# Kernel optimization log

Measured on AMD Instinct MI355X. Metric: run time of the kernel, lower is better.

The kernel has to match this reference:

```python
import jax, jax.numpy as jnp
import numpy as np

LN_EPS = 1e-5  # torch nn.LayerNorm default eps


def _layernorm(x, g, b):
    m = jnp.mean(x, -1, keepdims=True)
    v = jnp.mean((x - m) ** 2, -1, keepdims=True)
    return (x - m) / jnp.sqrt(v + LN_EPS) * g + b


def _dw_causal_conv(x, w, bias=None):
    # x: (B, L, C); w: (C, K) depthwise kernels; causal via left-pad K-1
    C = x.shape[-1]
    K = w.shape[-1]
    xt = jnp.swapaxes(x, 1, 2)                       # (B, C, L)
    xp = jnp.pad(xt, ((0, 0), (0, 0), (K - 1, 0)))
    y = jax.lax.conv_general_dilated(
        xp, w[:, None, :], (1,), 'VALID',
        feature_group_count=C, dimension_numbers=('NCH', 'OIH', 'NCH'))
    if bias is not None:
        y = y + bias[None, :, None]
    return jnp.swapaxes(y, 1, 2)                     # (B, L, C)


def _s4d(x, Bp, Cp, log_dt, Dp):
    # Diagonal SSM: kernel K[l] = sum_n C[n]*dB[n]*dA[n]^l, shared across channels
    L, Dm = x.shape[1], x.shape[2]
    n = Bp.shape[0]
    A = -jnp.arange(1, n + 1, dtype=x.dtype)
    dt = jnp.clip(jnp.exp(log_dt), 1e-4, 1.0)
    dA = jnp.exp(jnp.clip(dt * A, -10.0, 10.0))                  # (n,)
    dB = (dA - 1.0) / jnp.minimum(A, -1e-4) * Bp                 # (n,)
    pows = dA[:, None] ** jnp.arange(L, dtype=x.dtype)[None, :]  # (n, L)
    Kk = jnp.nan_to_num((Cp * dB) @ pows, nan=0.0, posinf=0.0, neginf=0.0)  # (L,)
    y = _dw_causal_conv(x, jnp.broadcast_to(Kk[None, :], (Dm, L)))
    return y + Dp * x


def _mamba_block(x, g, b, W_in, cw, cb, sB, sC, ldt, sD, W_out, rs):
    res = x
    h = _layernorm(x, g, b)
    xz = h @ W_in.T                                  # (B, L, 2*d_inner)
    xp, z = jnp.split(xz, 2, axis=-1)
    xc = _dw_causal_conv(xp, cw, cb)                 # depthwise causal conv, k=4
    y = _s4d(xc, sB, sC, ldt, sD) * jax.nn.sigmoid(z)
    y = y @ W_out.T
    return res + jnp.clip(rs, 0.0, 1.5) * y          # dropout is identity in eval


def _forward(spatial_tokens_init, pos_embed, ln_g, ln_b, W_in, conv_w, conv_b,
             ssm_B, ssm_C, log_dt, ssm_D, W_out, res_scale, fin_g, fin_b,
             imp_W1, imp_b1, imp_W2, imp_b2, tex_W, tex_b, edge_W, edge_b,
             str_W, str_b):
    x = spatial_tokens_init + pos_embed
    for i in range(ln_g.shape[0]):  # fixed small layer count
        x = _mamba_block(x, ln_g[i], ln_b[i], W_in[i], conv_w[i], conv_b[i],
                         ssm_B[i], ssm_C[i], log_dt[i], ssm_D[i], W_out[i],
                         res_scale[i])
    tokens = _layernorm(x, fin_g, fin_b)
    # F.normalize(dim=-1, eps=1e-6)
    tn = tokens / jnp.maximum(jnp.sqrt(jnp.sum(tokens ** 2, -1, keepdims=True)), 1e-6)
    h = jax.nn.gelu(tn @ imp_W1.T + imp_b1, approximate=False)
    logits = (h @ imp_W2.T + imp_b2)[..., 0]
    w = jax.nn.softmax(logits, axis=-1)
    feats = jnp.sum(tokens * w[..., None], axis=1)
    return (feats,
            feats @ tex_W.T + tex_b,
            feats @ edge_W.T + edge_b,
            feats @ str_W.T + str_b,
            tokens, w)


B, N, D, DI, NL, NS, KC, DH = 512, 256, 128, 256, 4, 16, 4, 64
H = D // 2


def setup_inputs() -> dict:
    ks = jax.random.split(jax.random.key(0), 26)
    r = lambda k, sh, s=0.02: jax.random.normal(k, sh, dtype=jnp.float32) * s
    inp = {
        'spatial_tokens_init': jax.random.normal(ks[0], (B, N, D), dtype=jnp.float32),
        'pos_embed': r(ks[1], (1, N, D)),
        'ln_g': jnp.ones((NL, D), jnp.float32),
        'ln_b': jnp.zeros((NL, D), jnp.float32),
        'W_in': r(ks[2], (NL, 2 * DI, D)),
        'conv_w': r(ks[3], (NL, DI, KC), 0.2),
        'conv_b': r(ks[4], (NL, DI), 0.02),
        'ssm_B': r(ks[5], (NL, NS)),
        'ssm_C': r(ks[6], (NL, NS)),
        'log_dt': jax.random.uniform(ks[7], (NL,), jnp.float32,
                                     minval=float(np.log(1e-3)), maxval=float(np.log(0.1))),
        'ssm_D': jnp.zeros((NL,), jnp.float32),
        'W_out': r(ks[8], (NL, D, DI)),
        'res_scale': jnp.ones((NL,), jnp.float32),
        'fin_g': jnp.ones((D,), jnp.float32),
        'fin_b': jnp.zeros((D,), jnp.float32),
        'imp_W1': r(ks[9], (H, D)),
        'imp_b1': jnp.zeros((H,), jnp.float32),
        'imp_W2': r(ks[10], (1, H)),
        'imp_b2': jnp.zeros((1,), jnp.float32),
        'tex_W': r(ks[11], (DH, D)),
        'tex_b': jnp.zeros((DH,), jnp.float32),
        'edge_W': r(ks[12], (DH, D)),
        'edge_b': jnp.zeros((DH,), jnp.float32),
        'str_W': r(ks[13], (DH, D)),
        'str_b': jnp.zeros((DH,), jnp.float32),
    }
    return inp


def reference(spatial_tokens_init, pos_embed, ln_g, ln_b, W_in, conv_w, conv_b,
              ssm_B, ssm_C, log_dt, ssm_D, W_out, res_scale, fin_g, fin_b,
              imp_W1, imp_b1, imp_W2, imp_b2, tex_W, tex_b, edge_W, edge_b,
              str_W, str_b):
    return _forward(spatial_tokens_init, pos_embed, ln_g, ln_b, W_in, conv_w,
                    conv_b, ssm_B, ssm_C, log_dt, ssm_D, W_out, res_scale,
                    fin_g, fin_b, imp_W1, imp_b1, imp_W2, imp_b2, tex_W, tex_b,
                    edge_W, edge_b, str_W, str_b)
```

## Files before the change

### kernel.cpp

```cpp
#include <hip/hip_runtime.h>
#include <hip/hip_bf16.h>


typedef __bf16 bf16_8 __attribute__((ext_vector_type(8)));
typedef __bf16 bf16_4 __attribute__((ext_vector_type(4)));
typedef float  f32_4  __attribute__((ext_vector_type(4)));

#define GLOAD16(src, dst) __builtin_amdgcn_global_load_lds( \
    (const __attribute__((address_space(1))) void*)(src),   \
    (__attribute__((address_space(3))) void*)(dst), 16, 0, 0)

__device__ __forceinline__ float fsig(float z) {
    float e = __expf(-z);
    return __builtin_amdgcn_rcpf(1.0f + e);
}

__global__ __launch_bounds__(256) void prep_kernel(const float* __restrict__ win,
                                                   const float* __restrict__ wout,
                                                   const float* __restrict__ w1,
                                                   __bf16* __restrict__ win16,
                                                   __bf16* __restrict__ wout16,
                                                   __bf16* __restrict__ w116) {
    int i = blockIdx.x * 256 + threadIdx.x;
    if (i < 4 * 512 * 128) win16[i] = (__bf16)win[i];
    if (i < 4 * 128 * 256) wout16[i] = (__bf16)wout[i];
    if (i < 64 * 128)      w116[i]  = (__bf16)w1[i];
}

__global__ __launch_bounds__(256) void build_T_kernel(const float* __restrict__ Bp,
                                                      const float* __restrict__ Cp,
                                                      const float* __restrict__ ldt,
                                                      const float* __restrict__ Dpv,
                                                      __bf16* __restrict__ Tg,
                                                      float* __restrict__ Rg) {
    __shared__ float rsum[4];
    int layer = blockIdx.y, l = blockIdx.x, j = threadIdx.x;
    int d = l - j;
    float val = 0.0f;
    if (d >= 0) {
        float dt = expf(ldt[layer]);
        dt = fminf(fmaxf(dt, 1e-4f), 1.0f);
        #pragma unroll
        for (int n = 0; n < 16; ++n) {
            float A = -(float)(n + 1);
            float e = fminf(fmaxf(dt * A, -10.0f), 10.0f);
            float dA = expf(e);
            float dB = (dA - 1.0f) / A * Bp[layer * 16 + n];
            val += Cp[layer * 16 + n] * dB * expf(e * (float)d);
        }
        if (d == 0) val += Dpv[layer];
    }
    __bf16 bv = (__bf16)val;
    Tg[layer * 65536 + l * 256 + j] = bv;
    float fv = (float)bv;
    #pragma unroll
    for (int o = 32; o; o >>= 1) fv += __shfl_xor(fv, o);
    int lane = j & 63, wave = j >> 6;
    if (lane == 0) rsum[wave] = fv;
    __syncthreads();
    if (j == 0) Rg[layer * 256 + l] = rsum[0] + rsum[1] + rsum[2] + rsum[3];
}

__global__ __launch_bounds__(256) void ln_first_kernel(const float4* __restrict__ init4,
                                                       const float4* __restrict__ pos4,
                                                       const float* __restrict__ g,
                                                       const float* __restrict__ bta,
                                                       float4* __restrict__ x4,
                                                       __bf16* __restrict__ h) {
    int tid = threadIdx.x;
    int wave = tid >> 6, lane = tid & 63;
    int half = lane >> 5, l32 = lane & 31;
    long tok = (long)blockIdx.x * 8 + wave * 2 + half;
    float4 v = init4[tok * 32 + l32];
    float4 p = pos4[(tok & 255) * 32 + l32];
    v.x += p.x; v.y += p.y; v.z += p.z; v.w += p.w;
    x4[tok * 32 + l32] = v;
    float s = v.x + v.y + v.z + v.w;
    float ss = v.x * v.x + v.y * v.y + v.z * v.z + v.w * v.w;
    #pragma unroll
    for (int o = 16; o; o >>= 1) { s += __shfl_xor(s, o); ss += __shfl_xor(ss, o); }
    float m = s * (1.0f / 128.0f);
    float var = ss * (1.0f / 128.0f) - m * m;
    float r = rsqrtf(var + 1e-5f);
    bf16_4 hv;
    int d0 = l32 * 4;
    hv[0] = (__bf16)((v.x - m) * r * g[d0]     + bta[d0]);
    hv[1] = (__bf16)((v.y - m) * r * g[d0 + 1] + bta[d0 + 1]);
    hv[2] = (__bf16)((v.z - m) * r * g[d0 + 2] + bta[d0 + 2]);
    hv[3] = (__bf16)((v.w - m) * r * g[d0 + 3] + bta[d0 + 3]);
    *(bf16_4*)(h + tok * 128 + d0) = hv;
}

__global__ __launch_bounds__(256) void gemm1_kernel(const __bf16* __restrict__ hmat,
                                                    const __bf16* __restrict__ win,
                                                    __bf16* __restrict__ xpt,
                                                    __bf16* __restrict__ z) {
    __shared__ __align__(16) __bf16 As[128 * 64];
    __shared__ __align__(16) __bf16 Bs[128 * 64];
    int tid = threadIdx.x;
    long m0 = (long)blockIdx.x * 128;
    int n0 = blockIdx.y * 128;
    int wave = tid >> 6, lane = tid & 63;
    int wm = wave >> 1, wn = wave & 1;
    int lrow = lane & 15, lk = (lane >> 4) * 8;
    int r7 = lrow & 7;
    int rl = lane >> 3, sl = lane & 7;
    int scol = ((sl ^ rl) << 3);
    f32_4 acc[4][4] = {};

    for (int kc = 0; kc < 2; ++kc) {
        const __bf16* asrc = hmat + m0 * 128 + kc * 64;
        const __bf16* bsrc = win + (long)n0 * 128 + kc * 64;
        #pragma unroll
        for (int j = 0; j < 4; ++j) {
            int chunk = wave * 4 + j;
            GLOAD16(asrc + (long)(chunk * 8 + rl) * 128 + scol, As + chunk * 512);
            GLOAD16(bsrc + (long)(chunk * 8 + rl) * 128 + scol, Bs + chunk * 512);
        }
        __syncthreads();
        #pragma unroll
        for (int kk = 0; kk < 64; kk += 32) {
            int sw = ((((kk + lk) >> 3) ^ r7) << 3);
            bf16_8 a[4], b[4];
            #pragma unroll
            for (int mt = 0; mt < 4; ++mt)
                a[mt] = *(const bf16_8*)(As + (wm * 64 + mt * 16 + lrow) * 64 + sw);
            #pragma unroll
            for (int nt = 0; nt < 4; ++nt)
                b[nt] = *(const bf16_8*)(Bs + (wn * 64 + nt * 16 + lrow) * 64 + sw);
            #pragma unroll
            for (int mt = 0; mt < 4; ++mt)
                #pragma unroll
                for (int nt = 0; nt < 4; ++nt)
                    acc[mt][nt] = __builtin_amdgcn_mfma_f32_16x16x32_bf16(
                        a[mt], b[nt], acc[mt][nt], 0, 0, 0);
        }
        __syncthreads();
    }

    int row_base = (lane >> 4) * 4;
    int col = lane & 15;
    if (n0 < 256) {
        #pragma unroll
        for (int mt = 0; mt < 4; ++mt) {
            long mg = m0 + wm * 64 + mt * 16 + row_base;
            int b = (int)(mg >> 8), l = (int)(mg & 255);
            #pragma unroll
            for (int nt = 0; nt < 4; ++nt) {
                int ng = n0 + wn * 64 + nt * 16 + col;
                bf16_4 o;
                #pragma unroll
                for (int r = 0; r < 4; ++r) o[r] = (__bf16)acc[mt][nt][r];
                *(bf16_4*)(xpt + (long)b * 65536 + (long)ng * 256 + l) = o;
            }
        }
    } else {
        int ncol0 = n0 - 256;
        #pragma unroll
        for (int mt = 0; mt < 4; ++mt) {
            long mg = m0 + wm * 64 + mt * 16 + row_base;
            #pragma unroll
            for (int nt = 0; nt < 4; ++nt) {
                int ng = ncol0 + wn * 64 + nt * 16 + col;
                #pragma unroll
                for (int r = 0; r < 4; ++r)
                    z[(mg + r) * 256 + ng] = (__bf16)acc[mt][nt][r];
            }
        }
    }
}

__global__ __launch_bounds__(512) void ssm_gemm_kernel(const __bf16* __restrict__ xct,
                                                       __bf16* __restrict__ zy,
                                                       const __bf16* __restrict__ Tg,
                                                       const float* __restrict__ Rg,
                                                       const float* __restrict__ cw,
                                                       const float* __restrict__ cb) {
    __shared__ __align__(16) __bf16 As[256 * 64];
    __shared__ __align__(16) __bf16 Bs[128 * 64];
    __shared__ float  bnd[3][128];
    __shared__ float  Rs[256];
    int tid = threadIdx.x;
    int batch = blockIdx.x >> 1;
    int ntile = blockIdx.x & 1;
    int c0 = ntile * 128;

    int wave = tid >> 6, lane = tid & 63;
    int wm = wave >> 2, wn = wave & 3;
    int lrow = lane & 15, lk = (lane >> 4) * 8;
    int r7 = lrow & 7;
    int quad = lane >> 4;
    int rl = lane >> 3, sl = lane & 7;
    int scol = ((sl ^ rl) << 3);
    f32_4 acc[8][2] = {};
    const __bf16* bsrc0 = xct + (long)batch * 65536 + (long)c0 * 256;

    if (tid < 256) Rs[tid] = Rg[tid];

    for (int kc = 0; kc < 4; ++kc) {
        int j0 = kc * 64;
        const __bf16* asrc = Tg + j0;
        const __bf16* bsrc = bsrc0 + j0;
        #pragma unroll
        for (int j = 0; j < 4; ++j) {
            int chunk = wave * 4 + j;
            GLOAD16(asrc + (long)(chunk * 8 + rl) * 256 + scol, As + chunk * 512);
        }
        #pragma unroll
        for (int j = 0; j < 2; ++j) {
            int chunk = wave * 2 + j;
            GLOAD16(bsrc + (long)(chunk * 8 + rl) * 256 + scol, Bs + chunk * 512);
        }
        __syncthreads();
        #pragma unroll
        for (int kk = 0; kk < 64; kk += 32) {
            int sw = ((((kk + lk) >> 3) ^ r7) << 3);
            bf16_8 b0 = *(const bf16_8*)(Bs + (wn * 32 + lrow) * 64 + sw);
            bf16_8 b1 = *(const bf16_8*)(Bs + (wn * 32 + 16 + lrow) * 64 + sw);
            #pragma unroll
            for (int mt = 0; mt < 8; ++mt) {
                bf16_8 a = *(const bf16_8*)(As + (wm * 128 + mt * 16 + lrow) * 64 + sw);
                acc[mt][0] = __builtin_amdgcn_mfma_f32_16x16x32_bf16(a, b0, acc[mt][0], 0, 0, 0);
                acc[mt][1] = __builtin_amdgcn_mfma_f32_16x16x32_bf16(a, b1, acc[mt][1], 0, 0, 0);
            }
        }
        __syncthreads();
    }

    if (wm == 0 && quad == 3) {
        #pragma unroll
        for (int nt = 0; nt < 2; ++nt) {
            int colb = wn * 32 + nt * 16 + lrow;
            bnd[0][colb] = acc[7][nt][1];
            bnd[1][colb] = acc[7][nt][2];
            bnd[2][colb] = acc[7][nt][3];
        }
    }
    __syncthreads();

    float4 wv[2]; float cbv[2];
    #pragma unroll
    for (int nt = 0; nt < 2; ++nt) {
        int cg = c0 + wn * 32 + nt * 16 + lrow;
        wv[nt] = *(const float4*)(cw + cg * 4);
        cbv[nt] = cb[cg];
    }
    int src = (lane + 48) & 63;

    #pragma unroll
    for (int mt = 0; mt < 8; ++mt) {
        int lbase = wm * 128 + mt * 16 + quad * 4;
        int mp = mt > 0 ? mt - 1 : 0;
        float R0 = Rs[lbase], R1 = Rs[lbase + 1], R2 = Rs[lbase + 2], R3 = Rs[lbase + 3];
        #pragma unroll
        for (int nt = 0; nt < 2; ++nt) {
            int colb = wn * 32 + nt * 16 + lrow;
            int cg = c0 + colb;
            float s1 = __shfl(acc[mt][nt][3], src);
            float s2 = __shfl(acc[mt][nt][2], src);
            float s3 = __shfl(acc[mt][nt][1], src);
            float t1, t2, t3;
            if (mt == 0) {
                if (wm == 1) { t1 = bnd[2][colb]; t2 = bnd[1][colb]; t3 = bnd[0][colb]; }
                else         { t1 = 0.0f; t2 = 0.0f; t3 = 0.0f; }
            } else {
                t1 = __shfl(acc[mp][nt][3], src);
                t2 = __shfl(acc[mp][nt][2], src);
                t3 = __shfl(acc[mp][nt][1], src);
            }
            float pm1 = quad ? s1 : t1;
            float pm2 = quad ? s2 : t2;
            float pm3 = quad ? s3 : t3;
            float p0 = acc[mt][nt][0], p1 = acc[mt][nt][1];
            float p2 = acc[mt][nt][2], p3 = acc[mt][nt][3];
            float y0 = wv[nt].x * pm3 + wv[nt].y * pm2 + wv[nt].z * pm1 + wv[nt].w * p0 + cbv[nt] * R0;
            float y1 = wv[nt].x * pm2 + wv[nt].y * pm1 + wv[nt].z * p0  + wv[nt].w * p1 + cbv[nt] * R1;
            float y2 = wv[nt].x * pm1 + wv[nt].y * p0  + wv[nt].z * p1  + wv[nt].w * p2 + cbv[nt] * R2;
            float y3 = wv[nt].x * p0  + wv[nt].y * p1  + wv[nt].z * p2  + wv[nt].w * p3 + cbv[nt] * R3;
            long base = (long)batch * 65536 + (long)lbase * 256 + cg;
            float z0 = (float)zy[base];
            float z1 = (float)zy[base + 256];
            float z2 = (float)zy[base + 512];
            float z3 = (float)zy[base + 768];
            zy[base]       = (__bf16)(y0 * fsig(z0));
            zy[base + 256] = (__bf16)(y1 * fsig(z1));
            zy[base + 512] = (__bf16)(y2 * fsig(z2));
            zy[base + 768] = (__bf16)(y3 * fsig(z3));
        }
    }
}

__global__ __launch_bounds__(256) void gemm2_kernel(const __bf16* __restrict__ y,
                                                    const __bf16* __restrict__ wout,
                                                    float* __restrict__ x,
                                                    const float* __restrict__ rs_p,
                                                    const float* __restrict__ g,
                                                    const float* __restrict__ bta,
                                                    __bf16* __restrict__ hout,
                                                    float* __restrict__ tokens_out,
                                                    int final_mode) {
    __shared__ __align__(16) __bf16 As[64 * 64];
    __shared__ __align__(16) __bf16 Bs[128 * 64];
    __shared__ float s_sum[64][2];
    __shared__ float s_ssq[64][2];
    int tid = threadIdx.x;
    long m0 = (long)blockIdx.x * 64;
    int wave = tid >> 6, lane = tid & 63;
    int wm = wave >> 1, wn = wave & 1;
    int lrow = lane & 15, lk = (lane >> 4) * 8;
    int r7 = lrow & 7;
    int rl = lane >> 3, sl = lane & 7;
    int scol = ((sl ^ rl) << 3);
    f32_4 acc[2][4] = {};

    for (int kc = 0; kc < 4; ++kc) {
        const __bf16* asrc = y + m0 * 256 + kc * 64;
        const __bf16* bsrc = wout + kc * 64;
        #pragma unroll
        for (int j = 0; j < 2; ++j) {
            int chunk = wave * 2 + j;
            GLOAD16(asrc + (long)(chunk * 8 + rl) * 256 + scol, As + chunk * 512);
        }
        #pragma unroll
        for (int j = 0; j < 4; ++j) {
            int chunk = wave * 4 + j;
            GLOAD16(bsrc + (long)(chunk * 8 + rl) * 256 + scol, Bs + chunk * 512);
        }
        __syncthreads();
        #pragma unroll
        for (int kk = 0; kk < 64; kk += 32) {
            int sw = ((((kk + lk) >> 3) ^ r7) << 3);
            bf16_8 a[2], b[4];
            #pragma unroll
            for (int mt = 0; mt < 2; ++mt)
                a[mt] = *(const bf16_8*)(As + (wm * 32 + mt * 16 + lrow) * 64 + sw);
            #pragma unroll
            for (int nt = 0; nt < 4; ++nt)
                b[nt] = *(const bf16_8*)(Bs + (wn * 64 + nt * 16 + lrow) * 64 + sw);
            #pragma unroll
            for (int mt = 0; mt < 2; ++mt)
                #pragma unroll
                for (int nt = 0; nt < 4; ++nt)
                    acc[mt][nt] = __builtin_amdgcn_mfma_f32_16x16x32_bf16(
                        a[mt], b[nt], acc[mt][nt], 0, 0, 0);
        }
        __syncthreads();
    }

    float rs = rs_p[0];
    rs = fminf(fmaxf(rs, 0.0f), 1.5f);
    int quad = lane >> 4;
    int col = lane & 15;

    #pragma unroll
    for (int mt = 0; mt < 2; ++mt) {
        int tb = wm * 32 + mt * 16 + quad * 4;
        long mg = m0 + tb;
        #pragma unroll
        for (int r = 0; r < 4; ++r) {
            float s = 0.0f, ss = 0.0f;
            #pragma unroll
            for (int nt = 0; nt < 4; ++nt) {
                int d = wn * 64 + nt * 16 + col;
                float xv = x[(mg + r) * 128 + d] + rs * acc[mt][nt][r];
                acc[mt][nt][r] = xv;
                s += xv; ss += xv * xv;
            }
            #pragma unroll
            for (int o = 8; o; o >>= 1) { s += __shfl_xor(s, o); ss += __shfl_xor(ss, o); }
            if (col == 0) {
                s_sum[tb + r][wn] = s;
                s_ssq[tb + r][wn] = ss;
            }
        }
    }
    __syncthreads();

    #pragma unroll
    for (int mt = 0; mt < 2; ++mt) {
        int tb = wm * 32 + mt * 16 + quad * 4;
        long mg = m0 + tb;
        #pragma unroll
        for (int r = 0; r < 4; ++r) {
            float s  = s_sum[tb + r][0] + s_sum[tb + r][1];
            float ss = s_ssq[tb + r][0] + s_ssq[tb + r][1];
            float m = s * (1.0f / 128.0f);
            float var = ss * (1.0f / 128.0f) - m * m;
            float rstd = rsqrtf(var + 1e-5f);
            #pragma unroll
            for (int nt = 0; nt < 4; ++nt) {
                int d = wn * 64 + nt * 16 + col;
                float xv = acc[mt][nt][r];
                x[(mg + r) * 128 + d] = xv;
                float t = (xv - m) * rstd * g[d] + bta[d];
                if (!final_mode) {
                    hout[(mg + r) * 128 + d] = (__bf16)t;
                } else {
                    tokens_out[(mg + r) * 128 + d] = t;
                }
            }
        }
    }
}

__global__ __launch_bounds__(256) void l2n_kernel(const float4* __restrict__ tokens4,
                                                  __bf16* __restrict__ tn) {
    int tid = threadIdx.x;
    int wave = tid >> 6, lane = tid & 63;
    int half = lane >> 5, l32 = lane & 31;
    long tok = (long)blockIdx.x * 8 + wave * 2 + half;
    float4 t = tokens4[tok * 32 + l32];
    float q = t.x * t.x + t.y * t.y + t.z * t.z + t.w * t.w;
    #pragma unroll
    for (int o = 16; o; o >>= 1) q += __shfl_xor(q, o);
    float inv = 1.0f / fmaxf(sqrtf(q), 1e-6f);
    bf16_4 o4;
    o4[0] = (__bf16)(t.x * inv); o4[1] = (__bf16)(t.y * inv);
    o4[2] = (__bf16)(t.z * inv); o4[3] = (__bf16)(t.w * inv);
    *(bf16_4*)(tn + tok * 128 + l32 * 4) = o4;
}

#define LDA 136
__global__ __launch_bounds__(256) void mlp_kernel(const __bf16* __restrict__ tn,
                                                  const __bf16* __restrict__ w1b,
                                                  const float* __restrict__ b1,
                                                  const float* __restrict__ W2,
                                                  const float* __restrict__ b2,
                                                  float* __restrict__ logits) {
    __shared__ __bf16 As[128 * LDA];
    __shared__ __bf16 Bs[64 * LDA];
    int tid = threadIdx.x;
    long m0 = (long)blockIdx.x * 128;
    const __bf16* asrc = tn + m0 * 128;
    #pragma unroll
    for (int i = 0; i < 8; ++i) {
        int idx = tid + i * 256;
        int row = idx >> 4, c = idx & 15;
        uint4 v = *(const uint4*)(asrc + row * 128 + c * 8);
        *(uint4*)(As + row * LDA + c * 8) = v;
    }
    #pragma unroll
    for (int i = 0; i < 4; ++i) {
        int idx = tid + i * 256;
        int row = idx >> 4, c = idx & 15;
        uint4 v = *(const uint4*)(w1b + row * 128 + c * 8);
        *(uint4*)(Bs + row * LDA + c * 8) = v;
    }
    __syncthreads();

    int wave = tid >> 6, lane = tid & 63;
    int lrow = lane & 15, lk = (lane >> 4) * 8;
    f32_4 acc[2][4] = {};
    #pragma unroll
    for (int kk = 0; kk < 128; kk += 32) {
        bf16_8 a[2], b[4];
        #pragma unroll
        for (int mt = 0; mt < 2; ++mt)
            a[mt] = *(const bf16_8*)(As + (wave * 32 + mt * 16 + lrow) * LDA + kk + lk);
        #pragma unroll
        for (int nt = 0; nt < 4; ++nt)
            b[nt] = *(const bf16_8*)(Bs + (nt * 16 + lrow) * LDA + kk + lk);
        #pragma unroll
        for (int mt = 0; mt < 2; ++mt)
            #pragma unroll
            for (int nt = 0; nt < 4; ++nt)
                acc[mt][nt] = __builtin_amdgcn_mfma_f32_16x16x32_bf16(
                    a[mt], b[nt], acc[mt][nt], 0, 0, 0);
    }

    int col = lane & 15, quad = lane >> 4;
    float b2v = b2[0];
    #pragma unroll
    for (int mt = 0; mt < 2; ++mt) {
        #pragma unroll
        for (int r = 0; r < 4; ++r) {
            float p = 0.0f;
            #pragma unroll
            for (int nt = 0; nt < 4; ++nt) {
                int jx = nt * 16 + col;
                float a = acc[mt][nt][r] + b1[jx];
                float gl = 0.5f * a * (1.0f + erff(a * 0.70710678118654752f));
                p += gl * W2[jx];
            }
            #pragma unroll
            for (int o = 8; o; o >>= 1) p += __shfl_xor(p, o);
            if (col == 0) {
                long tok = m0 + wave * 32 + mt * 16 + quad * 4 + r;
                logits[tok] = p + b2v;
            }
        }
    }
}

__global__ __launch_bounds__(256) void head_kernel(const float* __restrict__ tokens,
                                                   const float* __restrict__ logits,
                                                   const float* __restrict__ texW,
                                                   const float* __restrict__ texb,
                                                   const float* __restrict__ edgeW,
                                                   const float* __restrict__ edgeb,
                                                   const float* __restrict__ strW,
                                                   const float* __restrict__ strb,
                                                   float* __restrict__ feats_out,
                                                   float* __restrict__ tex_out,
                                                   float* __restrict__ edge_out,
                                                   float* __restrict__ str_out,
                                                   float* __restrict__ w_out) {
    __shared__ float wsm[256];
    __shared__ float red[8];
    __shared__ float feats_s[128];
    int b = blockIdx.x, tid = threadIdx.x;
    int lane = tid & 63, wave = tid >> 6;
    float lg = logits[(long)b * 256 + tid];
    float mx = lg;
    #pragma unroll
    for (int o = 32; o; o >>= 1) mx = fmaxf(mx, __shfl_xor(mx, o));
    if (lane == 0) red[wave] = mx;
    __syncthreads();
    float bm = fmaxf(fmaxf(red[0], red[1]), fmaxf(red[2], red[3]));
    float e = expf(lg - bm);
    float se = e;
    #pragma unroll
    for (int o = 32; o; o >>= 1) se += __shfl_xor(se, o);
    if (lane == 0) red[4 + wave] = se;
    __syncthreads();
    float tot = red[4] + red[5] + red[6] + red[7];
    float w = e / tot;
    wsm[tid] = w;
    w_out[(long)b * 256 + tid] = w;
    __syncthreads();
    if (tid < 128) {
        float acc = 0.0f;
        const float* tb = tokens + (long)b * 256 * 128 + tid;
        #pragma unroll 4
        for (int l = 0; l < 256; ++l) acc += tb[l * 128] * wsm[l];
        feats_s[tid] = acc;
        feats_out[(long)b * 128 + tid] = acc;
    }
    __syncthreads();
    if (tid < 192) {
        int head = tid >> 6, j = tid & 63;
        const float* W  = head == 0 ? texW : (head == 1 ? edgeW : strW);
        const float* bi = head == 0 ? texb : (head == 1 ? edgeb : strb);
        float* outp     = head == 0 ? tex_out : (head == 1 ? edge_out : str_out);
        const float* wr = W + j * 128;
        float acc = 0.0f;
        #pragma unroll 8
        for (int k = 0; k < 128; ++k) acc += feats_s[k] * wr[k];
        outp[(long)b * 64 + j] = acc + bi[j];
    }
}

extern "C" void kernel_launch(void* const* d_in, const int* in_sizes, int n_in,
                              void* d_out, int out_size, void* d_ws, size_t ws_size,
                              hipStream_t stream) {
    const float* init   = (const float*)d_in[0];
    const float* pos    = (const float*)d_in[1];
    const float* ln_g   = (const float*)d_in[2];
    const float* ln_b   = (const float*)d_in[3];
    const float* W_in   = (const float*)d_in[4];
    const float* conv_w = (const float*)d_in[5];
    const float* conv_b = (const float*)d_in[6];
    const float* ssm_B  = (const float*)d_in[7];
    const float* ssm_C  = (const float*)d_in[8];
    const float* log_dt = (const float*)d_in[9];
    const float* ssm_D  = (const float*)d_in[10];
    const float* W_out  = (const float*)d_in[11];
    const float* res_sc = (const float*)d_in[12];
    const float* fin_g  = (const float*)d_in[13];
    const float* fin_b  = (const float*)d_in[14];
    const float* imp_W1 = (const float*)d_in[15];
    const float* imp_b1 = (const float*)d_in[16];
    const float* imp_W2 = (const float*)d_in[17];
    const float* imp_b2 = (const float*)d_in[18];
    const float* tex_W  = (const float*)d_in[19];
    const float* tex_b  = (const float*)d_in[20];
    const float* edge_W = (const float*)d_in[21];
    const float* edge_b = (const float*)d_in[22];
    const float* str_W  = (const float*)d_in[23];
    const float* str_b  = (const float*)d_in[24];

    float* out = (float*)d_out;
    char* ws = (char*)d_ws;
    float*  x      = (float*)ws;
    __bf16* xpt    = (__bf16*)(ws + 67108864);
    __bf16* zb     = (__bf16*)(ws + 134217728);
    __bf16* hb     = (__bf16*)(ws + 201326592);
    __bf16* win16  = (__bf16*)(ws + 234881024);
    __bf16* wout16 = (__bf16*)(ws + 235405312);
    float*  logits = (float*)(ws + 235667456);
    __bf16* w1b    = (__bf16*)(ws + 236191744);
    __bf16* Tg     = (__bf16*)(ws + 236208128);
    float*  Rg     = (float*)(ws + 236732416);

    float* tokens = out + 163840;

    prep_kernel<<<1024, 256, 0, stream>>>(W_in, W_out, imp_W1, win16, wout16, w1b);
    build_T_kernel<<<dim3(256, 4), 256, 0, stream>>>(ssm_B, ssm_C, log_dt, ssm_D, Tg, Rg);
    ln_first_kernel<<<16384, 256, 0, stream>>>((const float4*)init, (const float4*)pos,
                                               ln_g, ln_b, (float4*)x, hb);
    for (int l = 0; l < 4; ++l) {
        gemm1_kernel<<<dim3(1024, 4), 256, 0, stream>>>(hb, win16 + l * 65536, xpt, zb);
        ssm_gemm_kernel<<<1024, 512, 0, stream>>>(xpt, zb, Tg + l * 65536, Rg + l * 256,
                                                  conv_w + l * 1024, conv_b + l * 256);
        int fin = (l == 3);
        const float* gn = fin ? fin_g : ln_g + (l + 1) * 128;
        const float* bn = fin ? fin_b : ln_b + (l + 1) * 128;
        gemm2_kernel<<<2048, 256, 0, stream>>>(zb, wout16 + l * 32768, x, res_sc + l,
                                               gn, bn, hb, fin ? tokens : nullptr, fin);
    }
    __bf16* tn = hb;
    l2n_kernel<<<16384, 256, 0, stream>>>((const float4*)tokens, tn);
    mlp_kernel<<<1024, 256, 0, stream>>>(tn, w1b, imp_b1, imp_W2, imp_b2, logits);
    head_kernel<<<512, 256, 0, stream>>>(tokens, logits, tex_W, tex_b, edge_W, edge_b,
                                         str_W, str_b, out, out + 65536, out + 98304,
                                         out + 131072, out + 16941056);
}
```

Baseline: 742.6 us.

## Load GEMM operands directly from global memory into registers, dropping LDS staging

```diff
diff --git a/kernel.cpp b/kernel.cpp
--- a/kernel.cpp
+++ b/kernel.cpp
@@ -5,10 +5,6 @@
 typedef __bf16 bf16_8 __attribute__((ext_vector_type(8)));
 typedef __bf16 bf16_4 __attribute__((ext_vector_type(4)));
 typedef float  f32_4  __attribute__((ext_vector_type(4)));
-
-#define GLOAD16(src, dst) __builtin_amdgcn_global_load_lds( \
-    (const __attribute__((address_space(1))) void*)(src),   \
-    (__attribute__((address_space(3))) void*)(dst), 16, 0, 0)
 
 __device__ __forceinline__ float fsig(float z) {
     float e = __expf(-z);
@@ -95,47 +91,31 @@
                                                     const __bf16* __restrict__ win,
                                                     __bf16* __restrict__ xpt,
                                                     __bf16* __restrict__ z) {
-    __shared__ __align__(16) __bf16 As[128 * 64];
-    __shared__ __align__(16) __bf16 Bs[128 * 64];
     int tid = threadIdx.x;
     long m0 = (long)blockIdx.x * 128;
     int n0 = blockIdx.y * 128;
     int wave = tid >> 6, lane = tid & 63;
     int wm = wave >> 1, wn = wave & 1;
     int lrow = lane & 15, lk = (lane >> 4) * 8;
-    int r7 = lrow & 7;
-    int rl = lane >> 3, sl = lane & 7;
-    int scol = ((sl ^ rl) << 3);
     f32_4 acc[4][4] = {};
 
-    for (int kc = 0; kc < 2; ++kc) {
-        const __bf16* asrc = hmat + m0 * 128 + kc * 64;
-        const __bf16* bsrc = win + (long)n0 * 128 + kc * 64;
-        #pragma unroll
-        for (int j = 0; j < 4; ++j) {
-            int chunk = wave * 4 + j;
-            GLOAD16(asrc + (long)(chunk * 8 + rl) * 128 + scol, As + chunk * 512);
-            GLOAD16(bsrc + (long)(chunk * 8 + rl) * 128 + scol, Bs + chunk * 512);
-        }
-        __syncthreads();
-        #pragma unroll
-        for (int kk = 0; kk < 64; kk += 32) {
-            int sw = ((((kk + lk) >> 3) ^ r7) << 3);
-            bf16_8 a[4], b[4];
-            #pragma unroll
-            for (int mt = 0; mt < 4; ++mt)
-                a[mt] = *(const bf16_8*)(As + (wm * 64 + mt * 16 + lrow) * 64 + sw);
+    const __bf16* abase = hmat + (m0 + wm * 64 + lrow) * 128 + lk;
+    const __bf16* bbase = win + (long)(n0 + wn * 64 + lrow) * 128 + lk;
+    #pragma unroll
+    for (int kk = 0; kk < 128; kk += 32) {
+        bf16_8 a[4], b[4];
+        #pragma unroll
+        for (int mt = 0; mt < 4; ++mt)
+            a[mt] = *(const bf16_8*)(abase + mt * 16 * 128 + kk);
+        #pragma unroll
+        for (int nt = 0; nt < 4; ++nt)
+            b[nt] = *(const bf16_8*)(bbase + nt * 16 * 128 + kk);
+        #pragma unroll
+        for (int mt = 0; mt < 4; ++mt)
             #pragma unroll
             for (int nt = 0; nt < 4; ++nt)
-                b[nt] = *(const bf16_8*)(Bs + (wn * 64 + nt * 16 + lrow) * 64 + sw);
-            #pragma unroll
-            for (int mt = 0; mt < 4; ++mt)
-                #pragma unroll
-                for (int nt = 0; nt < 4; ++nt)
-                    acc[mt][nt] = __builtin_amdgcn_mfma_f32_16x16x32_bf16(
-                        a[mt], b[nt], acc[mt][nt], 0, 0, 0);
-        }
-        __syncthreads();
+                acc[mt][nt] = __builtin_amdgcn_mfma_f32_16x16x32_bf16(
+                    a[mt], b[nt], acc[mt][nt], 0, 0, 0);
     }
 
     int row_base = (lane >> 4) * 4;
@@ -176,10 +156,8 @@
                                                        const float* __restrict__ Rg,
                                                        const float* __restrict__ cw,
                                                        const float* __restrict__ cb) {
-    __shared__ __align__(16) __bf16 As[256 * 64];
-    __shared__ __align__(16) __bf16 Bs[128 * 64];
-    __shared__ float  bnd[3][128];
-    __shared__ float  Rs[256];
+    __shared__ float bnd[3][128];
+    __shared__ float Rs[256];
     int tid = threadIdx.x;
     int batch = blockIdx.x >> 1;
     int ntile = blockIdx.x & 1;
@@ -188,43 +166,24 @@
     int wave = tid >> 6, lane = tid & 63;
     int wm = wave >> 2, wn = wave & 3;
     int lrow = lane & 15, lk = (lane >> 4) * 8;
-    int r7 = lrow & 7;
     int quad = lane >> 4;
-    int rl = lane >> 3, sl = lane & 7;
-    int scol = ((sl ^ rl) << 3);
     f32_4 acc[8][2] = {};
     const __bf16* bsrc0 = xct + (long)batch * 65536 + (long)c0 * 256;
 
     if (tid < 256) Rs[tid] = Rg[tid];
 
-    for (int kc = 0; kc < 4; ++kc) {
-        int j0 = kc * 64;
-        const __bf16* asrc = Tg + j0;
-        const __bf16* bsrc = bsrc0 + j0;
-        #pragma unroll
-        for (int j = 0; j < 4; ++j) {
-            int chunk = wave * 4 + j;
-            GLOAD16(asrc + (long)(chunk * 8 + rl) * 256 + scol, As + chunk * 512);
-        }
-        #pragma unroll
-        for (int j = 0; j < 2; ++j) {
-            int chunk = wave * 2 + j;
-            GLOAD16(bsrc + (long)(chunk * 8 + rl) * 256 + scol, Bs + chunk * 512);
-        }
-        __syncthreads();
-        #pragma unroll
-        for (int kk = 0; kk < 64; kk += 32) {
-            int sw = ((((kk + lk) >> 3) ^ r7) << 3);
-            bf16_8 b0 = *(const bf16_8*)(Bs + (wn * 32 + lrow) * 64 + sw);
-            bf16_8 b1 = *(const bf16_8*)(Bs + (wn * 32 + 16 + lrow) * 64 + sw);
-            #pragma unroll
-            for (int mt = 0; mt < 8; ++mt) {
-                bf16_8 a = *(const bf16_8*)(As + (wm * 128 + mt * 16 + lrow) * 64 + sw);
-                acc[mt][0] = __builtin_amdgcn_mfma_f32_16x16x32_bf16(a, b0, acc[mt][0], 0, 0, 0);
-                acc[mt][1] = __builtin_amdgcn_mfma_f32_16x16x32_bf16(a, b1, acc[mt][1], 0, 0, 0);
-            }
-        }
-        __syncthreads();
+    const __bf16* tbase = Tg + (wm * 128 + lrow) * 256 + lk;
+    const __bf16* bbase = bsrc0 + (long)(wn * 32 + lrow) * 256 + lk;
+    #pragma unroll
+    for (int kk = 0; kk < 256; kk += 32) {
+        bf16_8 b0 = *(const bf16_8*)(bbase + kk);
+        bf16_8 b1 = *(const bf16_8*)(bbase + 16 * 256 + kk);
+        #pragma unroll
+        for (int mt = 0; mt < 8; ++mt) {
+            bf16_8 a = *(const bf16_8*)(tbase + mt * 16 * 256 + kk);
+            acc[mt][0] = __builtin_amdgcn_mfma_f32_16x16x32_bf16(a, b0, acc[mt][0], 0, 0, 0);
+            acc[mt][1] = __builtin_amdgcn_mfma_f32_16x16x32_bf16(a, b1, acc[mt][1], 0, 0, 0);
+        }
     }
 
     if (wm == 0 && quad == 3) {
@@ -299,8 +258,6 @@
                                                     __bf16* __restrict__ hout,
                                                     float* __restrict__ tokens_out,
                                                     int final_mode) {
-    __shared__ __align__(16) __bf16 As[64 * 64];
-    __shared__ __align__(16) __bf16 Bs[128 * 64];
     __shared__ float s_sum[64][2];
     __shared__ float s_ssq[64][2];
     int tid = threadIdx.x;
@@ -308,43 +265,25 @@
     int wave = tid >> 6, lane = tid & 63;
     int wm = wave >> 1, wn = wave & 1;
     int lrow = lane & 15, lk = (lane >> 4) * 8;
-    int r7 = lrow & 7;
-    int rl = lane >> 3, sl = lane & 7;
-    int scol = ((sl ^ rl) << 3);
     f32_4 acc[2][4] = {};
 
-    for (int kc = 0; kc < 4; ++kc) {
-        const __bf16* asrc = y + m0 * 256 + kc * 64;
-        const __bf16* bsrc = wout + kc * 64;
-        #pragma unroll
-        for (int j = 0; j < 2; ++j) {
-            int chunk = wave * 2 + j;
-            GLOAD16(asrc + (long)(chunk * 8 + rl) * 256 + scol, As + chunk * 512);
-        }
-        #pragma unroll
-        for (int j = 0; j < 4; ++j) {
-            int chunk = wave * 4 + j;
-            GLOAD16(bsrc + (long)(chunk * 8 + rl) * 256 + scol, Bs + chunk * 512);
-        }
-        __syncthreads();
-        #pragma unroll
-        for (int kk = 0; kk < 64; kk += 32) {
-            int sw = ((((kk + lk) >> 3) ^ r7) << 3);
-            bf16_8 a[2], b[4];
-            #pragma unroll
-            for (int mt = 0; mt < 2; ++mt)
-                a[mt] = *(const bf16_8*)(As + (wm * 32 + mt * 16 + lrow) * 64 + sw);
+    const __bf16* abase = y + (m0 + wm * 32 + lrow) * 256 + lk;
+    const __bf16* bbase = wout + (wn * 64 + lrow) * 256 + lk;
+    #pragma unroll
+    for (int kk = 0; kk < 256; kk += 32) {
+        bf16_8 a[2], b[4];
+        #pragma unroll
+        for (int mt = 0; mt < 2; ++mt)
+            a[mt] = *(const bf16_8*)(abase + mt * 16 * 256 + kk);
+        #pragma unroll
+        for (int nt = 0; nt < 4; ++nt)
+            b[nt] = *(const bf16_8*)(bbase + nt * 16 * 256 + kk);
+        #pragma unroll
+        for (int mt = 0; mt < 2; ++mt)
             #pragma unroll
             for (int nt = 0; nt < 4; ++nt)
-                b[nt] = *(const bf16_8*)(Bs + (wn * 64 + nt * 16 + lrow) * 64 + sw);
-            #pragma unroll
-            for (int mt = 0; mt < 2; ++mt)
-                #pragma unroll
-                for (int nt = 0; nt < 4; ++nt)
-                    acc[mt][nt] = __builtin_amdgcn_mfma_f32_16x16x32_bf16(
-                        a[mt], b[nt], acc[mt][nt], 0, 0, 0);
-        }
-        __syncthreads();
+                acc[mt][nt] = __builtin_amdgcn_mfma_f32_16x16x32_bf16(
+                    a[mt], b[nt], acc[mt][nt], 0, 0, 0);
     }
 
     float rs = rs_p[0];
```

New measurement: 1.166 ms. 1.57x slower.
